# Kernel optimization log

Measured on AMD Instinct MI355X. Metric: run time of the kernel, lower is better.

The kernel has to match this reference:

```python
import jax, jax.numpy as jnp
import numpy as np
import math

N_STFT = 1025
N_MELS = 128
SAMPLE_RATE = 16000
F_MIN = 0.0
F_MAX = 8000.0
MAX_ITER = 20
LR = 0.3
MOMENTUM = 0.9
BATCH = 4
TIME = 1024


def _create_fb_matrix(n_freqs, f_min, f_max, n_mels, sample_rate):
    # Triangular mel filterbank, (n_freqs, n_mels), matching torchaudio's create_fb_matrix.
    all_freqs = np.linspace(0.0, sample_rate // 2, n_freqs)
    m_min = 2595.0 * math.log10(1.0 + f_min / 700.0)
    m_max = 2595.0 * math.log10(1.0 + f_max / 700.0)
    m_pts = np.linspace(m_min, m_max, n_mels + 2)
    f_pts = 700.0 * (10.0 ** (m_pts / 2595.0) - 1.0)
    f_diff = f_pts[1:] - f_pts[:-1]
    slopes = f_pts[None, :] - all_freqs[:, None]  # (n_freqs, n_mels+2)
    down_slopes = -slopes[:, :-2] / f_diff[:-1]
    up_slopes = slopes[:, 2:] / f_diff[1:]
    fb = np.maximum(0.0, np.minimum(down_slopes, up_slopes))
    return jnp.asarray(fb, dtype=jnp.float32)


def setup_inputs() -> dict:
    key = jax.random.key(0)
    k1, k2 = jax.random.split(key)
    melspec = jax.random.uniform(k1, (BATCH, N_MELS, TIME), dtype=jnp.float32)
    # torch.rand initialization of the estimated spectrogram, exposed for determinism
    spec_init = jax.random.uniform(k2, (BATCH, TIME, N_STFT), dtype=jnp.float32)
    fb = _create_fb_matrix(N_STFT, F_MIN, F_MAX, N_MELS, SAMPLE_RATE)
    return {"melspec": melspec, "spec_init": spec_init, "fb": fb}


def reference(melspec, spec_init, fb):
    # melspec: (B, n_mels, T) -> (B, T, n_mels); fb: (n_stft, n_mels)
    mel_t = jnp.swapaxes(melspec, -1, -2)
    b, t, _ = mel_t.shape
    inv = 2.0 / (b * t)  # d(mean over B*T of sum_m diff^2)/d(spec) prefactor

    def step(carry, _):
        spec, buf = carry
        diff = mel_t - jnp.einsum('btf,fm->btm', spec, fb)      # (B,T,M)
        grad = -inv * jnp.einsum('btm,fm->btf', diff, fb)       # (B,T,F)
        buf = MOMENTUM * buf + grad                              # SGD momentum buffer
        spec = jnp.maximum(spec - LR * buf, 0.0)                 # update + clamp(min=0)
        return (spec, buf), None

    init = (spec_init, jnp.zeros_like(spec_init))
    (spec, _), _ = jax.lax.scan(step, init, None, length=MAX_ITER)
    return jnp.swapaxes(spec, -1, -2)  # (B, n_stft, T)
```

## Files before the change

kernel.cpp:

```cpp
#include <hip/hip_runtime.h>

#define N_STFT 1025
#define N_MELS 128
#define BATCH 4
#define TIME 1024
#define MAX_ITER 20

typedef unsigned long long u64;
typedef unsigned int u32;

__global__ void imel_prep(const float* __restrict__ fb, int* __restrict__ m0f,
                          float* __restrict__ w0a, float* __restrict__ w1a) {
  const int w = threadIdx.x >> 6, l = threadIdx.x & 63;
  const int f = blockIdx.x * 4 + w;
  if (f >= N_STFT) return;
  const float* row = fb + (size_t)f * N_MELS;
  const unsigned long long mlo = __ballot(row[l] != 0.0f);
  const unsigned long long mhi = __ballot(row[l + 64] != 0.0f);
  if (l == 0) {
    int m0 = mlo ? __builtin_ctzll(mlo)
                 : (mhi ? 64 + __builtin_ctzll(mhi) : 0);
    if (m0 > N_MELS - 2) m0 = N_MELS - 2;
    m0f[f] = m0;
    w0a[f] = row[m0];
    w1a[f] = row[m0 + 1];
  }
}

__device__ __forceinline__ u64 pk_rn(float x, float y) {
  return (u64)(u32)__float2int_rn(x) | ((u64)(u32)__float2int_rn(y) << 32);
}

__global__ __launch_bounds__(256, 2) void imel_main(
    const float* __restrict__ melspec, const float* __restrict__ spec_init,
    const int* __restrict__ m0f, const float* __restrict__ w0a,
    const float* __restrict__ w1a, float* __restrict__ out) {
  __shared__ u64   s_P[4][N_MELS];
  __shared__ float s_mel[8][N_MELS];
  __shared__ float s_out[8][1060];

  const int tid = threadIdx.x;
  const int w   = tid >> 6;
  const int l   = tid & 63;
  const int flat = (blockIdx.x & 7) * 64 + (blockIdx.x >> 3);
  const int b   = flat >> 7;
  const int t0  = (flat & 127) << 3;
  const int tA  = t0 + 2 * w;

  for (int i = tid; i < 8 * N_MELS; i += 256) {
    const int m = i >> 3, r = i & 7;
    s_mel[r][m] = melspec[((size_t)b * N_MELS + m) * TIME + t0 + r];
  }
  __syncthreads();

  const float SCALE  = 16777216.0f;
  const float GRAD_N = -2.0f / (BATCH * TIME);
  const float C2 = (2.0f / (BATCH * TIME)) * 3.5527136788005009e-15f;

  float rsA[16], rsB[16], rbA[16], rbB[16];
  float rw0[16], rw1[16], ccA[16], ccB[16];
  int rm[16];

  const float* srowA = spec_init + (size_t)(b * TIME + tA) * N_STFT;
  const float* srowB = srowA + N_STFT;
  const float* melA = &s_mel[2 * w][0];
  const float* melB = &s_mel[2 * w + 1][0];
#pragma unroll
  for (int k = 0; k < 16; ++k) {
    const int f = (l << 4) + k;
    rsA[k] = srowA[f];
    rsB[k] = srowB[f];
    const int m = m0f[f];
    rm[k] = m;
    const float w0 = w0a[f], w1 = w1a[f];
    rw0[k] = w0 * SCALE;
    rw1[k] = w1 * SCALE;
    ccA[k] = GRAD_N * fmaf(melA[m], w0, melA[m + 1] * w1);
    ccB[k] = GRAD_N * fmaf(melB[m], w0, melB[m + 1] * w1);
    rbA[k] = 0.f;
    rbB[k] = 0.f;
  }
  const float rtA = (l == 63) ? srowA[1024] : 0.f;
  const float rtB = (l == 63) ? srowB[1024] : 0.f;

  bool adv[16];
  adv[0] = false;
#pragma unroll
  for (int k = 1; k < 16; ++k) adv[k] = (rm[k] != rm[k - 1]);

  u64* __restrict__ Pw = &s_P[w][0];
  Pw[l] = 0ULL;
  Pw[l + 64] = 0ULL;

  for (int it = 0; it < MAX_ITER; ++it) {
    {
      float a0A = rsA[0] * rw0[0], a1A = rsA[0] * rw1[0];
      float a0B = rsB[0] * rw0[0], a1B = rsB[0] * rw1[0];
#pragma unroll
      for (int k = 1; k < 16; ++k) {
        if (adv[k]) atomicAdd(&Pw[rm[k - 1]], pk_rn(a0A, a0B));
        const float n0A = (adv[k] ? a1A : a0A) + rsA[k] * rw0[k];
        a1A = (adv[k] ? 0.f : a1A) + rsA[k] * rw1[k];
        a0A = n0A;
        const float n0B = (adv[k] ? a1B : a0B) + rsB[k] * rw0[k];
        a1B = (adv[k] ? 0.f : a1B) + rsB[k] * rw1[k];
        a0B = n0B;
      }
      atomicAdd(&Pw[rm[15]],     pk_rn(a0A, a0B));
      atomicAdd(&Pw[rm[15] + 1], pk_rn(a1A, a1B));
    }
    __builtin_amdgcn_wave_barrier();
#pragma unroll
    for (int k = 0; k < 16; ++k) {
      const u64 q0 = Pw[rm[k]];
      const u64 q1 = Pw[rm[k] + 1];
      const float p0A = (float)(int)(u32)q0;
      const float p0B = (float)(int)(u32)(q0 >> 32);
      const float p1A = (float)(int)(u32)q1;
      const float p1B = (float)(int)(u32)(q1 >> 32);
      const float gA = fmaf(fmaf(p1A, rw1[k], p0A * rw0[k]), C2, ccA[k]);
      const float gB = fmaf(fmaf(p1B, rw1[k], p0B * rw0[k]), C2, ccB[k]);
      rbA[k] = fmaf(0.9f, rbA[k], gA);
      rbB[k] = fmaf(0.9f, rbB[k], gB);
      rsA[k] = fmaxf(fmaf(-0.3f, rbA[k], rsA[k]), 0.f);
      rsB[k] = fmaxf(fmaf(-0.3f, rbB[k], rsB[k]), 0.f);
    }
    __builtin_amdgcn_wave_barrier();
    Pw[l] = 0ULL;
    Pw[l + 64] = 0ULL;
    __builtin_amdgcn_wave_barrier();
  }

#pragma unroll
  for (int k = 0; k < 16; ++k) {
    const int f = (l << 4) + k;
    s_out[2 * w][f + (f >> 5)]     = rsA[k];
    s_out[2 * w + 1][f + (f >> 5)] = rsB[k];
  }
  if (l == 63) {
    s_out[2 * w][1056]     = rtA;
    s_out[2 * w + 1][1056] = rtB;
  }
  __syncthreads();

  const int tl = tid & 7;
  const int fg = tid >> 3;
  float* obase = out + (size_t)b * N_STFT * TIME + t0 + tl;
  for (int f = fg; f < N_STFT; f += 32) {
    obase[(size_t)f * TIME] = s_out[tl][f + (f >> 5)];
  }
}

extern "C" void kernel_launch(void* const* d_in, const int* in_sizes, int n_in,
                              void* d_out, int out_size, void* d_ws, size_t ws_size,
                              hipStream_t stream) {
  const float* melspec = (const float*)d_in[0];
  const float* spec_init = (const float*)d_in[1];
  const float* fb = (const float*)d_in[2];
  float* out = (float*)d_out;

  int* m0f = (int*)d_ws;
  float* w0a = (float*)((char*)d_ws + 5120);
  float* w1a = (float*)((char*)d_ws + 10240);

  imel_prep<<<dim3(257), dim3(256), 0, stream>>>(fb, m0f, w0a, w1a);
  imel_main<<<dim3(512), dim3(256), 0, stream>>>(melspec, spec_init, m0f, w0a, w1a, out);
}
```

Measured before the change: 117.4 us.

## Use one time row per wave with float LDS atomics instead of packed fixed-point

Each wave now handles a single time row instead of two, so blocks grow to 512 threads (8 waves) and register pressure per thread drops by half. The packed 64-bit fixed-point integer atomics that combined two rows are replaced by plain float LDS atomicAdd, with the gradient constants folded into one learning-rate scale. This aims to raise occupancy and remove the float-to-int packing and conversion work, at the cost of twice as many atomic operations per row pair. Float atomics also make accumulation order nondeterministic.

```diff
diff --git a/kernel.cpp b/kernel.cpp
--- a/kernel.cpp
+++ b/kernel.cpp
@@ -5,9 +5,6 @@
 #define BATCH 4
 #define TIME 1024
 #define MAX_ITER 20
-
-typedef unsigned long long u64;
-typedef unsigned int u32;
 
 __global__ void imel_prep(const float* __restrict__ fb, int* __restrict__ m0f,
                           float* __restrict__ w0a, float* __restrict__ w1a) {
@@ -27,15 +24,11 @@
   }
 }
 
-__device__ __forceinline__ u64 pk_rn(float x, float y) {
-  return (u64)(u32)__float2int_rn(x) | ((u64)(u32)__float2int_rn(y) << 32);
-}
-
-__global__ __launch_bounds__(256, 2) void imel_main(
+__global__ __launch_bounds__(512, 4) void imel_main(
     const float* __restrict__ melspec, const float* __restrict__ spec_init,
     const int* __restrict__ m0f, const float* __restrict__ w0a,
     const float* __restrict__ w1a, float* __restrict__ out) {
-  __shared__ u64   s_P[4][N_MELS];
+  __shared__ float s_P[8][N_MELS];
   __shared__ float s_mel[8][N_MELS];
   __shared__ float s_out[8][1060];
 
@@ -45,108 +38,80 @@
   const int flat = (blockIdx.x & 7) * 64 + (blockIdx.x >> 3);
   const int b   = flat >> 7;
   const int t0  = (flat & 127) << 3;
-  const int tA  = t0 + 2 * w;
+  const int tA  = t0 + w;
 
-  for (int i = tid; i < 8 * N_MELS; i += 256) {
+  for (int i = tid; i < 8 * N_MELS; i += 512) {
     const int m = i >> 3, r = i & 7;
     s_mel[r][m] = melspec[((size_t)b * N_MELS + m) * TIME + t0 + r];
   }
   __syncthreads();
 
-  const float SCALE  = 16777216.0f;
-  const float GRAD_N = -2.0f / (BATCH * TIME);
-  const float C2 = (2.0f / (BATCH * TIME)) * 3.5527136788005009e-15f;
+  const float LRI = 0.3f * (2.0f / (BATCH * TIME));
 
-  float rsA[16], rsB[16], rbA[16], rbB[16];
-  float rw0[16], rw1[16], ccA[16], ccB[16];
+  float rs[16], rb[16], rw0[16], rw1[16], cc[16];
   int rm[16];
 
-  const float* srowA = spec_init + (size_t)(b * TIME + tA) * N_STFT;
-  const float* srowB = srowA + N_STFT;
-  const float* melA = &s_mel[2 * w][0];
-  const float* melB = &s_mel[2 * w + 1][0];
+  const float* srow = spec_init + (size_t)(b * TIME + tA) * N_STFT;
+  const float* melW = &s_mel[w][0];
 #pragma unroll
   for (int k = 0; k < 16; ++k) {
     const int f = (l << 4) + k;
-    rsA[k] = srowA[f];
-    rsB[k] = srowB[f];
+    rs[k] = srow[f];
     const int m = m0f[f];
     rm[k] = m;
     const float w0 = w0a[f], w1 = w1a[f];
-    rw0[k] = w0 * SCALE;
-    rw1[k] = w1 * SCALE;
-    ccA[k] = GRAD_N * fmaf(melA[m], w0, melA[m + 1] * w1);
-    ccB[k] = GRAD_N * fmaf(melB[m], w0, melB[m + 1] * w1);
-    rbA[k] = 0.f;
-    rbB[k] = 0.f;
+    rw0[k] = w0;
+    rw1[k] = w1;
+    cc[k] = -fmaf(melW[m], w0, melW[m + 1] * w1);
+    rb[k] = 0.f;
   }
-  const float rtA = (l == 63) ? srowA[1024] : 0.f;
-  const float rtB = (l == 63) ? srowB[1024] : 0.f;
+  const float rt = (l == 63) ? srow[1024] : 0.f;
 
-  bool adv[16];
-  adv[0] = false;
-#pragma unroll
-  for (int k = 1; k < 16; ++k) adv[k] = (rm[k] != rm[k - 1]);
-
-  u64* __restrict__ Pw = &s_P[w][0];
-  Pw[l] = 0ULL;
-  Pw[l + 64] = 0ULL;
+  float* __restrict__ Pw = &s_P[w][0];
+  Pw[l] = 0.f;
+  Pw[l + 64] = 0.f;
 
   for (int it = 0; it < MAX_ITER; ++it) {
     {
-      float a0A = rsA[0] * rw0[0], a1A = rsA[0] * rw1[0];
-      float a0B = rsB[0] * rw0[0], a1B = rsB[0] * rw1[0];
+      float a0 = rs[0] * rw0[0], a1 = rs[0] * rw1[0];
 #pragma unroll
       for (int k = 1; k < 16; ++k) {
-        if (adv[k]) atomicAdd(&Pw[rm[k - 1]], pk_rn(a0A, a0B));
-        const float n0A = (adv[k] ? a1A : a0A) + rsA[k] * rw0[k];
-        a1A = (adv[k] ? 0.f : a1A) + rsA[k] * rw1[k];
-        a0A = n0A;
-        const float n0B = (adv[k] ? a1B : a0B) + rsB[k] * rw0[k];
-        a1B = (adv[k] ? 0.f : a1B) + rsB[k] * rw1[k];
-        a0B = n0B;
+        const bool adv = (rm[k] != rm[k - 1]);
+        if (adv) atomicAdd(&Pw[rm[k - 1]], a0);
+        const float n0 = (adv ? a1 : a0) + rs[k] * rw0[k];
+        a1 = (adv ? 0.f : a1) + rs[k] * rw1[k];
+        a0 = n0;
       }
-      atomicAdd(&Pw[rm[15]],     pk_rn(a0A, a0B));
-      atomicAdd(&Pw[rm[15] + 1], pk_rn(a1A, a1B));
+      atomicAdd(&Pw[rm[15]],     a0);
+      atomicAdd(&Pw[rm[15] + 1], a1);
     }
     __builtin_amdgcn_wave_barrier();
 #pragma unroll
     for (int k = 0; k < 16; ++k) {
-      const u64 q0 = Pw[rm[k]];
-      const u64 q1 = Pw[rm[k] + 1];
-      const float p0A = (float)(int)(u32)q0;
-      const float p0B = (float)(int)(u32)(q0 >> 32);
-      const float p1A = (float)(int)(u32)q1;
-      const float p1B = (float)(int)(u32)(q1 >> 32);
-      const float gA = fmaf(fmaf(p1A, rw1[k], p0A * rw0[k]), C2, ccA[k]);
-      const float gB = fmaf(fmaf(p1B, rw1[k], p0B * rw0[k]), C2, ccB[k]);
-      rbA[k] = fmaf(0.9f, rbA[k], gA);
-      rbB[k] = fmaf(0.9f, rbB[k], gB);
-      rsA[k] = fmaxf(fmaf(-0.3f, rbA[k], rsA[k]), 0.f);
-      rsB[k] = fmaxf(fmaf(-0.3f, rbB[k], rsB[k]), 0.f);
+      const float p0 = Pw[rm[k]];
+      const float p1 = Pw[rm[k] + 1];
+      const float g = fmaf(p0, rw0[k], fmaf(p1, rw1[k], cc[k]));
+      rb[k] = fmaf(0.9f, rb[k], g);
+      rs[k] = fmaxf(fmaf(-LRI, rb[k], rs[k]), 0.f);
     }
     __builtin_amdgcn_wave_barrier();
-    Pw[l] = 0ULL;
-    Pw[l + 64] = 0ULL;
+    Pw[l] = 0.f;
+    Pw[l + 64] = 0.f;
     __builtin_amdgcn_wave_barrier();
   }
 
 #pragma unroll
   for (int k = 0; k < 16; ++k) {
     const int f = (l << 4) + k;
-    s_out[2 * w][f + (f >> 5)]     = rsA[k];
-    s_out[2 * w + 1][f + (f >> 5)] = rsB[k];
+    s_out[w][f + (f >> 5)] = rs[k];
   }
-  if (l == 63) {
-    s_out[2 * w][1056]     = rtA;
-    s_out[2 * w + 1][1056] = rtB;
-  }
+  if (l == 63) s_out[w][1056] = rt;
   __syncthreads();
 
   const int tl = tid & 7;
   const int fg = tid >> 3;
   float* obase = out + (size_t)b * N_STFT * TIME + t0 + tl;
-  for (int f = fg; f < N_STFT; f += 32) {
+  for (int f = fg; f < N_STFT; f += 64) {
     obase[(size_t)f * TIME] = s_out[tl][f + (f >> 5)];
   }
 }
@@ -164,5 +129,5 @@
   float* w1a = (float*)((char*)d_ws + 10240);
 
   imel_prep<<<dim3(257), dim3(256), 0, stream>>>(fb, m0f, w0a, w1a);
-  imel_main<<<dim3(512), dim3(256), 0, stream>>>(melspec, spec_init, m0f, w0a, w1a, out);
+  imel_main<<<dim3(512), dim3(512), 0, stream>>>(melspec, spec_init, m0f, w0a, w1a, out);
 }
```

Result: slower. 204.4 us (+74.2%).
